# Performance work log

Hardware: AMD Instinct MI355X
Metric: run time of the kernel (lower is better)

The kernel has to match this reference:

```python
import jax, jax.numpy as jnp
import numpy as np

NUM_CLASSES = [5, 7, 4, 6, 3, 8, 5, 4, 6, 7, 3, 5, 4, 6, 8, 5, 7, 4, 6, 3]
N_ONE_HOTS = 20
N_OTHERS = 30
H = 48
W = 48
B = 128
N_MAP = 32
ENC_OUT = 32
RES_C = 128
OH_EMB = 9
SUM_NC = sum(NUM_CLASSES)  # 106


def conv2d(x, w, b=None, pad=0):
    # x: NCHW, w: OIHW
    y = jax.lax.conv_general_dilated(
        x, w, window_strides=(1, 1), padding=[(pad, pad), (pad, pad)],
        dimension_numbers=('NCHW', 'OIHW', 'NCHW'))
    if b is not None:
        y = y + b[None, :, None, None]
    return y


def setup_inputs() -> dict:
    key = jax.random.key(0)
    ks = jax.random.split(key, 20)
    x = jax.random.normal(ks[0], (B, 1 + N_MAP, H, W), dtype=jnp.float32)
    # first N_ONE_HOTS entries of flattened channel 0 are categorical indices
    idx_cols = [jax.random.randint(jax.random.fold_in(ks[1], j), (B,), 0, nc)
                for j, nc in enumerate(NUM_CLASSES)]
    idx = jnp.stack(idx_cols, axis=1).astype(jnp.float32)  # (B, 20)
    x = x.at[:, 0, 0, :N_ONE_HOTS].set(idx)
    s = 0.05
    inp = {
        'x': x,
        'fc_w': jax.random.normal(ks[2], (OH_EMB, SUM_NC), jnp.float32) * s,
        'fc_b': jnp.zeros((OH_EMB,), jnp.float32),
        'oh_conv_w': jax.random.normal(ks[3], (OH_EMB, OH_EMB, 1, 1), jnp.float32) * s,
        'oh_conv_b': jnp.zeros((OH_EMB,), jnp.float32),
        'others_conv_w': jax.random.normal(ks[4], (N_OTHERS, N_OTHERS, 1, 1), jnp.float32) * s,
        'others_conv_b': jnp.zeros((N_OTHERS,), jnp.float32),
        'all_conv_w': jax.random.normal(ks[5], (ENC_OUT, OH_EMB + N_OTHERS, 1, 1), jnp.float32) * s,
        'all_conv_b': jnp.zeros((ENC_OUT,), jnp.float32),
        'conv1_w': jax.random.normal(ks[6], (RES_C, ENC_OUT + N_MAP, 1, 1), jnp.float32) * s,
        'conv1_b': jnp.zeros((RES_C,), jnp.float32),
        'rconv1_w': jax.random.normal(ks[7], (RES_C, RES_C, 5, 5), jnp.float32) * s,
        'rconv1_b': jnp.zeros((RES_C,), jnp.float32),
        'rconv2_w': jax.random.normal(ks[8], (RES_C, RES_C, 5, 5), jnp.float32) * s,
        'rconv2_b': jnp.zeros((RES_C,), jnp.float32),
        'se_w1': jax.random.normal(ks[9], (RES_C // 16, RES_C), jnp.float32) * s,
        'se_w2': jax.random.normal(ks[10], (RES_C, RES_C // 16), jnp.float32) * s,
    }
    return inp


def reference(x, fc_w, fc_b, oh_conv_w, oh_conv_b, others_conv_w, others_conv_b,
              all_conv_w, all_conv_b, conv1_w, conv1_b, rconv1_w, rconv1_b,
              rconv2_w, rconv2_b, se_w1, se_w2):
    b = x.shape[0]
    gi = x[:, 0].reshape(b, -1)                 # (b, H*W)
    map_feature = x[:, 1:]                      # (b, N_MAP, H, W)
    idx = jax.lax.stop_gradient(gi[:, :N_ONE_HOTS]).astype(jnp.int32)
    others = gi[:, N_ONE_HOTS:N_ONE_HOTS + N_OTHERS]   # (b, 30)
    # vectorized one-hot build (replaces the quadratic python loop)
    oh = jnp.concatenate(
        [jax.nn.one_hot(idx[:, j], nc, dtype=x.dtype) for j, nc in enumerate(NUM_CLASSES)],
        axis=1)                                 # (b, SUM_NC)
    v = oh @ fc_w.T + fc_b                      # (b, 9)
    # faithful torch expand((h,w)+shape).reshape((b,-1,h,w)) semantics
    v = jnp.broadcast_to(v, (H, W, b, OH_EMB)).reshape(b, OH_EMB, H, W)
    o = jnp.broadcast_to(others, (H, W, b, N_OTHERS)).reshape(b, N_OTHERS, H, W)
    v = conv2d(v, oh_conv_w, oh_conv_b)
    o = conv2d(o, others_conv_w, others_conv_b)
    gi_map = conv2d(jnp.concatenate([v, o], axis=1), all_conv_w, all_conv_b)  # (b, 32, H, W)
    h = conv2d(jnp.concatenate([gi_map, map_feature], axis=1), conv1_w, conv1_b)  # (b, 128, H, W)
    # residual block: 5x5 convs, LeakyReLU, SE, identity skip (in==out)
    identity = h
    y = jax.nn.leaky_relu(conv2d(h, rconv1_w, rconv1_b, pad=2))
    y = conv2d(y, rconv2_w, rconv2_b, pad=2)
    s = y.mean(axis=(2, 3))                     # (b, 128)
    s = jax.nn.sigmoid(jax.nn.relu(s @ se_w1.T) @ se_w2.T)
    y = y * s[:, :, None, None]
    return jax.nn.leaky_relu(y + identity)
```

## Files before the change

kernel.cpp:

```cpp
#include <hip/hip_runtime.h>
#include <hip/hip_bf16.h>
#include <cstddef>

#define HH 48
#define WW 48
#define PIX 2304
#define PPIX 2704
#define BB 128
#define RESC 128
#define XCH 33

typedef short bf16x8 __attribute__((ext_vector_type(8)));
typedef float f32x4 __attribute__((ext_vector_type(4)));

static __device__ __forceinline__ float b2f(unsigned short u) {
    unsigned x = ((unsigned)u) << 16;
    return __builtin_bit_cast(float, x);
}
static __device__ __forceinline__ unsigned short f2b(float f) {
    __hip_bfloat16 hb = __float2bfloat16(f);
    return __builtin_bit_cast(unsigned short, hb);
}

#define GLOAD_LDS16(gp, lp) __builtin_amdgcn_global_load_lds( \
    (const __attribute__((address_space(1))) void*)(gp), \
    (__attribute__((address_space(3))) void*)(lp), 16, 0, 0)

__global__ void k_compute_v(const float* __restrict__ x, const float* __restrict__ fc_w,
                            const float* __restrict__ fc_b, float* __restrict__ v) {
    int b = blockIdx.x * blockDim.x + threadIdx.x;
    if (b >= BB) return;
    const int off[20] = {0,5,12,16,22,25,33,38,42,48,55,58,63,67,73,81,86,93,97,103};
    const float* gi = x + (size_t)b * XCH * PIX;
    int cols[20];
    #pragma unroll
    for (int j = 0; j < 20; j++) cols[j] = off[j] + (int)gi[j];
    #pragma unroll
    for (int e = 0; e < 9; e++) {
        float acc = fc_b[e];
        #pragma unroll
        for (int j = 0; j < 20; j++) acc += fc_w[e * 106 + cols[j]];
        v[b * 9 + e] = acc;
    }
}

__global__ void k_compute_G(const float* __restrict__ x, const float* __restrict__ v,
                            const float* __restrict__ ohw, const float* __restrict__ ohb,
                            const float* __restrict__ otw, const float* __restrict__ otb,
                            const float* __restrict__ aw,  const float* __restrict__ ab,
                            const float* __restrict__ c1w, const float* __restrict__ c1b,
                            float* __restrict__ G) {
    int p = blockIdx.x * blockDim.x + threadIdx.x;
    if (p >= PIX) return;
    float sv = v[((p / 9) & 127) * 9 + (p % 9)];
    float om[30];
    #pragma unroll
    for (int c2 = 0; c2 < 30; c2++) {
        int tmp = c2 * 24 + p;
        int c = tmp % 30;
        int bb = (c2 * 76 + tmp / 30) & 127;
        om[c2] = x[(size_t)bb * XCH * PIX + 20 + c];
    }
    float v9[9];
    #pragma unroll
    for (int e = 0; e < 9; e++) {
        float srow = 0.f;
        #pragma unroll
        for (int e2 = 0; e2 < 9; e2++) srow += ohw[e * 9 + e2];
        v9[e] = ohb[e] + srow * sv;
    }
    float o30[30];
    #pragma unroll
    for (int c = 0; c < 30; c++) {
        float a = otb[c];
        #pragma unroll
        for (int c2 = 0; c2 < 30; c2++) a += otw[c * 30 + c2] * om[c2];
        o30[c] = a;
    }
    float gi32[32];
    #pragma unroll
    for (int g = 0; g < 32; g++) {
        float a = ab[g];
        #pragma unroll
        for (int e = 0; e < 9; e++) a += aw[g * 39 + e] * v9[e];
        #pragma unroll
        for (int c = 0; c < 30; c++) a += aw[g * 39 + 9 + c] * o30[c];
        gi32[g] = a;
    }
    for (int oc = 0; oc < 128; oc++) {
        float a = c1b[oc];
        #pragma unroll
        for (int g = 0; g < 32; g++) a += c1w[oc * 64 + g] * gi32[g];
        G[p * 128 + oc] = a;
    }
}

__global__ void k_convert_w(const float* __restrict__ w1, const float* __restrict__ w2,
                            __hip_bfloat16* __restrict__ wb1, __hip_bfloat16* __restrict__ wb2) {
    int i = blockIdx.x * 256 + threadIdx.x;
    if (i >= 25 * 128 * 128) return;
    int tap = i / 16384, r = i % 16384;
    int oc = r >> 7, ic = r & 127;
    size_t src = (size_t)(oc * 128 + ic) * 25 + tap;
    wb1[i] = __float2bfloat16(w1[src]);
    wb2[i] = __float2bfloat16(w2[src]);
}

__global__ void k_zero_border(__hip_bfloat16* __restrict__ a, __hip_bfloat16* __restrict__ b2) {
    int img = blockIdx.x, t = threadIdx.x;
    for (int j = t; j < 6400; j += 256) {
        int pb = j >> 4, c16 = j & 15;
        int y, x2;
        if (pb < 208) { int q = pb / 52; y = q < 2 ? q : q + 48; x2 = pb % 52; }
        else { int r = pb - 208; y = 2 + (r >> 2); int c = r & 3; x2 = c < 2 ? c : c + 48; }
        size_t off = ((size_t)img * PPIX + y * 52 + x2) * 128 + c16 * 8;
        uint4 z = {0, 0, 0, 0};
        *(uint4*)(a + off) = z;
        *(uint4*)(b2 + off) = z;
    }
}

__global__ __launch_bounds__(256) void k_conv1(const float* __restrict__ x, const float* __restrict__ c1w,
                                               const float* __restrict__ G, __hip_bfloat16* __restrict__ h) {
    __shared__ float xm[32][64];
    __shared__ float w1[32][128];
    int b = blockIdx.y, p0 = blockIdx.x * 64;
    int t = threadIdx.x;
    for (int i = t; i < 4096; i += 256) { int m = i >> 7, oc = i & 127; w1[m][oc] = c1w[oc * 64 + 32 + m]; }
    for (int i = t; i < 2048; i += 256) {
        int m = i >> 6, pix = i & 63;
        xm[m][pix] = x[(size_t)b * XCH * PIX + (size_t)(1 + m) * PIX + p0 + pix];
    }
    __syncthreads();
    int pix = t & 63, ocg = t >> 6;
    float acc[32] = {};
    for (int m = 0; m < 32; m++) {
        float xv = xm[m][pix];
        const float4* wr = (const float4*)&w1[m][ocg * 32];
        #pragma unroll
        for (int k4 = 0; k4 < 8; k4++) {
            float4 wv = wr[k4];
            acc[k4 * 4 + 0] += wv.x * xv; acc[k4 * 4 + 1] += wv.y * xv;
            acc[k4 * 4 + 2] += wv.z * xv; acc[k4 * 4 + 3] += wv.w * xv;
        }
    }
    int p = p0 + pix;
    int py = p / 48, px2 = p % 48;
    size_t hb = ((size_t)b * PPIX + (py + 2) * 52 + px2 + 2) * 128 + ocg * 32;
    const float* gp = &G[(size_t)p * 128 + ocg * 32];
    #pragma unroll
    for (int q = 0; q < 4; q++) {
        unsigned short u[8];
        #pragma unroll
        for (int j = 0; j < 8; j++) u[j] = f2b(acc[q * 8 + j] + gp[q * 8 + j]);
        *(uint4*)(&h[hb + q * 8]) = *(uint4*)u;
    }
}

template<bool LEAKY, bool MEAN, bool PADOUT>
__global__ __launch_bounds__(256, 2) void k_conv5_mfma(
        const __hip_bfloat16* __restrict__ in,
        const __hip_bfloat16* __restrict__ w,
        const float* __restrict__ bias,
        __hip_bfloat16* __restrict__ out,
        float* __restrict__ mean) {
    __shared__ __align__(16) char lds[2][25600];
    int b = blockIdx.z, tile = blockIdx.x;
    int ty0 = (tile / 3) * 16, tx0 = (tile % 3) * 16;
    int t = threadIdx.x, lane = t & 63, wave = t >> 6;
    int wm = wave & 1, wn = wave >> 1;
    int l15 = lane & 15, lg = lane >> 4;

    const size_t inb = (size_t)b * PPIX * 128;
    const __hip_bfloat16* wbase = w + (size_t)(wm * 64 + l15) * 128 + lg * 8;

    int sbase[8];
    #pragma unroll
    for (int n = 0; n < 8; ++n) sbase[n] = (wn * 8 + n) * 20 + l15;

    f32x4 acc[4][8] = {};

    auto stage = [&](int buf, int icb2) {
        #pragma unroll
        for (int k = 0; k < 6; ++k) {
            int sg = k * 256 + t;
            int u = sg >> 3, j = sg & 7;
            int bb = j ^ (u & 7);
            int s = (u << 1) | (bb >> 2);
            int lg2 = bb & 3;
            int ry = s / 20, rx = s % 20;
            const __hip_bfloat16* gp = in + inb + (size_t)((ty0 + ry) * 52 + tx0 + rx) * 128 + icb2 + lg2 * 8;
            char* lp = &lds[buf][(k * 256 + (wave << 6)) * 16];
            GLOAD_LDS16(gp, lp);
        }
        if (wave == 0) {
            int sg = 1536 + lane;
            int u = sg >> 3, j = sg & 7;
            int bb = j ^ (u & 7);
            int s = (u << 1) | (bb >> 2);
            int lg2 = bb & 3;
            int ry = s / 20, rx = s % 20;
            const __hip_bfloat16* gp = in + inb + (size_t)((ty0 + ry) * 52 + tx0 + rx) * 128 + icb2 + lg2 * 8;
            char* lp = &lds[buf][1536 * 16];
            GLOAD_LDS16(gp, lp);
        }
    };

#define AISSUE(Areg, tap_) do { \
        const __hip_bfloat16* wp = wbase + (size_t)(tap_) * 16384 + icb; \
        Areg[0] = *(const bf16x8*)(wp); \
        Areg[1] = *(const bf16x8*)(wp + 2048); \
        Areg[2] = *(const bf16x8*)(wp + 4096); \
        Areg[3] = *(const bf16x8*)(wp + 6144); \
    } while (0)

#define CTAP(Areg, tap_) do { \
        int toff = (tap_) + 15 * ((tap_) / 5); \
        __builtin_amdgcn_s_setprio(1); \
        _Pragma("unroll") \
        for (int n = 0; n < 8; ++n) { \
            int s = sbase[n] + toff; \
            int u = s >> 1; \
            int jj = (((s & 1) << 2) | lg) ^ (u & 7); \
            bf16x8 Bv = *(const bf16x8*)(cb + (u << 7) + (jj << 4)); \
            acc[0][n] = __builtin_amdgcn_mfma_f32_16x16x32_bf16(Areg[0], Bv, acc[0][n], 0, 0, 0); \
            acc[1][n] = __builtin_amdgcn_mfma_f32_16x16x32_bf16(Areg[1], Bv, acc[1][n], 0, 0, 0); \
            acc[2][n] = __builtin_amdgcn_mfma_f32_16x16x32_bf16(Areg[2], Bv, acc[2][n], 0, 0, 0); \
            acc[3][n] = __builtin_amdgcn_mfma_f32_16x16x32_bf16(Areg[3], Bv, acc[3][n], 0, 0, 0); \
        } \
        __builtin_amdgcn_s_setprio(0); \
    } while (0)

    stage(0, 0);
    __syncthreads();

    for (int c = 0; c < 4; ++c) {
        const int icb = c * 32;
        const char* cb = lds[c & 1];
        bf16x8 A0[4], A1[4];
        AISSUE(A0, 0);
        AISSUE(A1, 1);
        __builtin_amdgcn_sched_barrier(0);
        if (c < 3) stage((c + 1) & 1, icb + 32);
        __builtin_amdgcn_sched_barrier(0);
        for (int i = 0; i < 12; ++i) {
            int tp = 2 * i;
            CTAP(A0, tp);
            AISSUE(A0, tp + 2);
            CTAP(A1, tp + 1);
            AISSUE(A1, tp + 3);
        }
        CTAP(A0, 24);
        if (c < 3) __syncthreads();
    }
#undef AISSUE
#undef CTAP

    #pragma unroll
    for (int m = 0; m < 4; ++m) {
        int ocm = wm * 64 + m * 16 + lg * 4;
        float b0 = bias[ocm], b1 = bias[ocm + 1], b2 = bias[ocm + 2], b3 = bias[ocm + 3];
        float ps0 = 0, ps1 = 0, ps2 = 0, ps3 = 0;
        #pragma unroll
        for (int n = 0; n < 8; ++n) {
            float v0 = acc[m][n][0] + b0, v1 = acc[m][n][1] + b1;
            float v2 = acc[m][n][2] + b2, v3 = acc[m][n][3] + b3;
            ps0 += v0; ps1 += v1; ps2 += v2; ps3 += v3;
            if (LEAKY) {
                v0 = v0 > 0.f ? v0 : 0.01f * v0; v1 = v1 > 0.f ? v1 : 0.01f * v1;
                v2 = v2 > 0.f ? v2 : 0.01f * v2; v3 = v3 > 0.f ? v3 : 0.01f * v3;
            }
            int row = ty0 + wn * 8 + n, col = tx0 + l15;
            size_t off;
            if (PADOUT) off = ((size_t)b * PPIX + (row + 2) * 52 + col + 2) * 128 + ocm;
            else        off = ((size_t)b * PIX + row * 48 + col) * 128 + ocm;
            uint2 pk;
            pk.x = (unsigned)f2b(v0) | ((unsigned)f2b(v1) << 16);
            pk.y = (unsigned)f2b(v2) | ((unsigned)f2b(v3) << 16);
            *(uint2*)(out + off) = pk;
        }
        if (MEAN) {
            #pragma unroll
            for (int mask = 1; mask < 16; mask <<= 1) {
                ps0 += __shfl_xor(ps0, mask);
                ps1 += __shfl_xor(ps1, mask);
                ps2 += __shfl_xor(ps2, mask);
                ps3 += __shfl_xor(ps3, mask);
            }
            if (l15 == 0) {
                atomicAdd(&mean[b * 128 + ocm], ps0);
                atomicAdd(&mean[b * 128 + ocm + 1], ps1);
                atomicAdd(&mean[b * 128 + ocm + 2], ps2);
                atomicAdd(&mean[b * 128 + ocm + 3], ps3);
            }
        }
    }
}

__global__ void k_se(const float* __restrict__ mean, const float* __restrict__ w1,
                     const float* __restrict__ w2, float* __restrict__ s) {
    __shared__ float m[128];
    __shared__ float tt[8];
    int b = blockIdx.x, t = threadIdx.x;
    m[t] = mean[b * RESC + t] * (1.0f / 2304.0f);
    __syncthreads();
    if (t < 8) {
        float a = 0.f;
        for (int i = 0; i < 128; i++) a += w1[t * 128 + i] * m[i];
        tt[t] = a > 0.f ? a : 0.f;
    }
    __syncthreads();
    float a = 0.f;
    #pragma unroll
    for (int r = 0; r < 8; r++) a += w2[t * 8 + r] * tt[r];
    s[b * RESC + t] = 1.f / (1.f + expf(-a));
}

__global__ __launch_bounds__(256) void k_final(const __hip_bfloat16* __restrict__ y2,
                                               const __hip_bfloat16* __restrict__ h,
                                               const float* __restrict__ sg, float* __restrict__ out) {
    __shared__ float sl[128];
    __shared__ float tile[64 * 129];
    int b = blockIdx.y, p0 = blockIdx.x * 64, t = threadIdx.x;
    if (t < 128) sl[t] = sg[b * 128 + t];
    __syncthreads();
    #pragma unroll
    for (int k = 0; k < 4; ++k) {
        int j = t + k * 256;
        int pix = j >> 4, c = j & 15;
        int p = p0 + pix;
        int py = p / 48, px2 = p % 48;
        uint4 yv = *(const uint4*)(y2 + ((size_t)b * PIX + p) * 128 + c * 8);
        uint4 hv = *(const uint4*)(h + ((size_t)b * PPIX + (py + 2) * 52 + px2 + 2) * 128 + c * 8);
        const unsigned short* yp = (const unsigned short*)&yv;
        const unsigned short* hp = (const unsigned short*)&hv;
        #pragma unroll
        for (int jj = 0; jj < 8; ++jj) {
            int oc = c * 8 + jj;
            tile[pix * 129 + oc] = b2f(yp[jj]) * sl[oc] + b2f(hp[jj]);
        }
    }
    __syncthreads();
    int oc = t >> 1, xh = (t & 1) * 32;
    float ov[32];
    #pragma unroll
    for (int i = 0; i < 32; ++i) {
        float v = tile[(xh + i) * 129 + oc];
        ov[i] = v > 0.f ? v : 0.01f * v;
    }
    float* op = out + ((size_t)b * 128 + oc) * PIX + p0 + xh;
    #pragma unroll
    for (int q = 0; q < 8; ++q) ((float4*)op)[q] = *(float4*)&ov[q * 4];
}

extern "C" void kernel_launch(void* const* d_in, const int* in_sizes, int n_in,
                              void* d_out, int out_size, void* d_ws, size_t ws_size,
                              hipStream_t stream) {
    const float* x      = (const float*)d_in[0];
    const float* fc_w   = (const float*)d_in[1];
    const float* fc_b   = (const float*)d_in[2];
    const float* ohw    = (const float*)d_in[3];
    const float* ohb    = (const float*)d_in[4];
    const float* otw    = (const float*)d_in[5];
    const float* otb    = (const float*)d_in[6];
    const float* aw     = (const float*)d_in[7];
    const float* ab     = (const float*)d_in[8];
    const float* c1w    = (const float*)d_in[9];
    const float* c1b    = (const float*)d_in[10];
    const float* r1w    = (const float*)d_in[11];
    const float* r1b    = (const float*)d_in[12];
    const float* r2w    = (const float*)d_in[13];
    const float* r2b    = (const float*)d_in[14];
    const float* se_w1  = (const float*)d_in[15];
    const float* se_w2  = (const float*)d_in[16];

    const size_t padb = (size_t)BB * PPIX * 128 * sizeof(__hip_bfloat16);
    char* ws = (char*)d_ws;
    __hip_bfloat16* h    = (__hip_bfloat16*)ws;  ws += padb;
    __hip_bfloat16* y1   = (__hip_bfloat16*)ws;  ws += padb;
    __hip_bfloat16* y2   = (__hip_bfloat16*)ws;  ws += (size_t)BB * PIX * 128 * sizeof(__hip_bfloat16);
    float* G    = (float*)ws;                    ws += (size_t)PIX * 128 * sizeof(float);
    float* v    = (float*)ws;                    ws += (size_t)BB * 9 * sizeof(float);
    __hip_bfloat16* wb1 = (__hip_bfloat16*)ws;   ws += (size_t)25 * 128 * 128 * sizeof(__hip_bfloat16);
    __hip_bfloat16* wb2 = (__hip_bfloat16*)ws;   ws += (size_t)25 * 128 * 128 * sizeof(__hip_bfloat16);
    ws += 131072;
    float* mean = (float*)ws;                    ws += (size_t)BB * RESC * sizeof(float);
    float* sgate= (float*)ws;                    ws += (size_t)BB * RESC * sizeof(float);

    k_compute_v<<<1, 128, 0, stream>>>(x, fc_w, fc_b, v);
    k_compute_G<<<9, 256, 0, stream>>>(x, v, ohw, ohb, otw, otb, aw, ab, c1w, c1b, G);
    k_convert_w<<<1600, 256, 0, stream>>>(r1w, r2w, wb1, wb2);
    k_zero_border<<<128, 256, 0, stream>>>(h, y1);
    k_conv1<<<dim3(36, 128), 256, 0, stream>>>(x, c1w, G, h);
    k_conv5_mfma<true, false, true><<<dim3(9, 1, 128), 256, 0, stream>>>(h, wb1, r1b, y1, nullptr);
    hipMemsetAsync(mean, 0, (size_t)BB * RESC * sizeof(float), stream);
    k_conv5_mfma<false, true, false><<<dim3(9, 1, 128), 256, 0, stream>>>(y1, wb2, r2b, y2, mean);
    k_se<<<128, 128, 0, stream>>>(mean, se_w1, se_w2, sgate);
    k_final<<<dim3(36, 128), 256, 0, stream>>>(y2, h, sgate, (float*)d_out);
}
```

Measured before the change: 812.8 us.

## Halve conv5 spatial tile to 8x16 and raise occupancy to four blocks

Result: slower. 1.562 ms (+92.2%).

```diff
diff --git a/kernel.cpp b/kernel.cpp
--- a/kernel.cpp
+++ b/kernel.cpp
@@ -158,103 +158,79 @@
 }
 
 template<bool LEAKY, bool MEAN, bool PADOUT>
-__global__ __launch_bounds__(256, 2) void k_conv5_mfma(
+__global__ __launch_bounds__(256, 4) void k_conv5_mfma(
         const __hip_bfloat16* __restrict__ in,
         const __hip_bfloat16* __restrict__ w,
         const float* __restrict__ bias,
         __hip_bfloat16* __restrict__ out,
         float* __restrict__ mean) {
-    __shared__ __align__(16) char lds[2][25600];
+    __shared__ __align__(16) char lds[2 * 15360];
     int b = blockIdx.z, tile = blockIdx.x;
-    int ty0 = (tile / 3) * 16, tx0 = (tile % 3) * 16;
+    int ty0 = (tile / 3) * 8, tx0 = (tile % 3) * 16;
     int t = threadIdx.x, lane = t & 63, wave = t >> 6;
-    int wm = wave & 1, wn = wave >> 1;
+    int wm = wave & 1, wp = wave >> 1;
     int l15 = lane & 15, lg = lane >> 4;
 
     const size_t inb = (size_t)b * PPIX * 128;
-    const __hip_bfloat16* wbase = w + (size_t)(wm * 64 + l15) * 128 + lg * 8;
-
-    int sbase[8];
-    #pragma unroll
-    for (int n = 0; n < 8; ++n) sbase[n] = (wn * 8 + n) * 20 + l15;
-
-    f32x4 acc[4][8] = {};
+    const int wrow = (wm * 64 + l15) * 128 + lg * 8;
+
+    int sbase[4];
+    #pragma unroll
+    for (int n = 0; n < 4; ++n) sbase[n] = (wp * 4 + n) * 20 + l15;
+
+    f32x4 acc[4][4] = {};
 
     auto stage = [&](int buf, int icb2) {
         #pragma unroll
-        for (int k = 0; k < 6; ++k) {
-            int sg = k * 256 + t;
-            int u = sg >> 3, j = sg & 7;
-            int bb = j ^ (u & 7);
-            int s = (u << 1) | (bb >> 2);
-            int lg2 = bb & 3;
-            int ry = s / 20, rx = s % 20;
-            const __hip_bfloat16* gp = in + inb + (size_t)((ty0 + ry) * 52 + tx0 + rx) * 128 + icb2 + lg2 * 8;
-            char* lp = &lds[buf][(k * 256 + (wave << 6)) * 16];
-            GLOAD_LDS16(gp, lp);
-        }
-        if (wave == 0) {
-            int sg = 1536 + lane;
-            int u = sg >> 3, j = sg & 7;
-            int bb = j ^ (u & 7);
-            int s = (u << 1) | (bb >> 2);
-            int lg2 = bb & 3;
-            int ry = s / 20, rx = s % 20;
-            const __hip_bfloat16* gp = in + inb + (size_t)((ty0 + ry) * 52 + tx0 + rx) * 128 + icb2 + lg2 * 8;
-            char* lp = &lds[buf][1536 * 16];
-            GLOAD_LDS16(gp, lp);
+        for (int k = 0; k < 4; ++k) {
+            if (k < 3 || t < 192) {
+                int sg = k * 256 + t;
+                int u = sg >> 3, j = sg & 7;
+                int bb = j ^ (u & 7);
+                int s = (u << 1) | (bb >> 2);
+                int lg2 = bb & 3;
+                int ry = s / 20, rx = s % 20;
+                const __hip_bfloat16* gp = in + inb + (size_t)((ty0 + ry) * 52 + tx0 + rx) * 128 + icb2 + lg2 * 8;
+                char* lp = lds + buf * 15360 + sg * 16;
+                GLOAD_LDS16(gp, lp);
+            }
         }
     };
 
-#define AISSUE(Areg, tap_) do { \
-        const __hip_bfloat16* wp = wbase + (size_t)(tap_) * 16384 + icb; \
-        Areg[0] = *(const bf16x8*)(wp); \
-        Areg[1] = *(const bf16x8*)(wp + 2048); \
-        Areg[2] = *(const bf16x8*)(wp + 4096); \
-        Areg[3] = *(const bf16x8*)(wp + 6144); \
-    } while (0)
-
-#define CTAP(Areg, tap_) do { \
-        int toff = (tap_) + 15 * ((tap_) / 5); \
-        __builtin_amdgcn_s_setprio(1); \
-        _Pragma("unroll") \
-        for (int n = 0; n < 8; ++n) { \
-            int s = sbase[n] + toff; \
-            int u = s >> 1; \
-            int jj = (((s & 1) << 2) | lg) ^ (u & 7); \
-            bf16x8 Bv = *(const bf16x8*)(cb + (u << 7) + (jj << 4)); \
-            acc[0][n] = __builtin_amdgcn_mfma_f32_16x16x32_bf16(Areg[0], Bv, acc[0][n], 0, 0, 0); \
-            acc[1][n] = __builtin_amdgcn_mfma_f32_16x16x32_bf16(Areg[1], Bv, acc[1][n], 0, 0, 0); \
-            acc[2][n] = __builtin_amdgcn_mfma_f32_16x16x32_bf16(Areg[2], Bv, acc[2][n], 0, 0, 0); \
-            acc[3][n] = __builtin_amdgcn_mfma_f32_16x16x32_bf16(Areg[3], Bv, acc[3][n], 0, 0, 0); \
-        } \
-        __builtin_amdgcn_s_setprio(0); \
-    } while (0)
-
     stage(0, 0);
     __syncthreads();
 
+    #pragma unroll 1
     for (int c = 0; c < 4; ++c) {
         const int icb = c * 32;
-        const char* cb = lds[c & 1];
-        bf16x8 A0[4], A1[4];
-        AISSUE(A0, 0);
-        AISSUE(A1, 1);
-        __builtin_amdgcn_sched_barrier(0);
-        if (c < 3) stage((c + 1) & 1, icb + 32);
-        __builtin_amdgcn_sched_barrier(0);
-        for (int i = 0; i < 12; ++i) {
-            int tp = 2 * i;
-            CTAP(A0, tp);
-            AISSUE(A0, tp + 2);
-            CTAP(A1, tp + 1);
-            AISSUE(A1, tp + 3);
-        }
-        CTAP(A0, 24);
+        const char* cb = lds + (c & 1) * 15360;
+        #pragma unroll
+        for (int dy = 0; dy < 5; ++dy) {
+            #pragma unroll
+            for (int dx = 0; dx < 5; ++dx) {
+                const __hip_bfloat16* wt = w + (size_t)(dy * 5 + dx) * 16384 + wrow + icb;
+                bf16x8 A0 = *(const bf16x8*)(wt);
+                bf16x8 A1 = *(const bf16x8*)(wt + 2048);
+                bf16x8 A2 = *(const bf16x8*)(wt + 4096);
+                bf16x8 A3 = *(const bf16x8*)(wt + 6144);
+                if (dy == 0 && dx == 2 && c < 3) stage((c + 1) & 1, icb + 32);
+                __builtin_amdgcn_s_setprio(1);
+                #pragma unroll
+                for (int n = 0; n < 4; ++n) {
+                    int s = sbase[n] + dy * 20 + dx;
+                    int u = s >> 1;
+                    int jj = (((s & 1) << 2) | lg) ^ (u & 7);
+                    bf16x8 Bv = *(const bf16x8*)(cb + (u << 7) + (jj << 4));
+                    acc[0][n] = __builtin_amdgcn_mfma_f32_16x16x32_bf16(A0, Bv, acc[0][n], 0, 0, 0);
+                    acc[1][n] = __builtin_amdgcn_mfma_f32_16x16x32_bf16(A1, Bv, acc[1][n], 0, 0, 0);
+                    acc[2][n] = __builtin_amdgcn_mfma_f32_16x16x32_bf16(A2, Bv, acc[2][n], 0, 0, 0);
+                    acc[3][n] = __builtin_amdgcn_mfma_f32_16x16x32_bf16(A3, Bv, acc[3][n], 0, 0, 0);
+                }
+                __builtin_amdgcn_s_setprio(0);
+            }
+        }
         if (c < 3) __syncthreads();
     }
-#undef AISSUE
-#undef CTAP
 
     #pragma unroll
     for (int m = 0; m < 4; ++m) {
@@ -262,7 +238,7 @@
         float b0 = bias[ocm], b1 = bias[ocm + 1], b2 = bias[ocm + 2], b3 = bias[ocm + 3];
         float ps0 = 0, ps1 = 0, ps2 = 0, ps3 = 0;
         #pragma unroll
-        for (int n = 0; n < 8; ++n) {
+        for (int n = 0; n < 4; ++n) {
             float v0 = acc[m][n][0] + b0, v1 = acc[m][n][1] + b1;
             float v2 = acc[m][n][2] + b2, v3 = acc[m][n][3] + b3;
             ps0 += v0; ps1 += v1; ps2 += v2; ps3 += v3;
@@ -270,7 +246,7 @@
                 v0 = v0 > 0.f ? v0 : 0.01f * v0; v1 = v1 > 0.f ? v1 : 0.01f * v1;
                 v2 = v2 > 0.f ? v2 : 0.01f * v2; v3 = v3 > 0.f ? v3 : 0.01f * v3;
             }
-            int row = ty0 + wn * 8 + n, col = tx0 + l15;
+            int row = ty0 + wp * 4 + n, col = tx0 + l15;
             size_t off;
             if (PADOUT) off = ((size_t)b * PPIX + (row + 2) * 52 + col + 2) * 128 + ocm;
             else        off = ((size_t)b * PIX + row * 48 + col) * 128 + ocm;
@@ -383,7 +359,6 @@
     float* v    = (float*)ws;                    ws += (size_t)BB * 9 * sizeof(float);
     __hip_bfloat16* wb1 = (__hip_bfloat16*)ws;   ws += (size_t)25 * 128 * 128 * sizeof(__hip_bfloat16);
     __hip_bfloat16* wb2 = (__hip_bfloat16*)ws;   ws += (size_t)25 * 128 * 128 * sizeof(__hip_bfloat16);
-    ws += 131072;
     float* mean = (float*)ws;                    ws += (size_t)BB * RESC * sizeof(float);
     float* sgate= (float*)ws;                    ws += (size_t)BB * RESC * sizeof(float);
 
@@ -392,9 +367,9 @@
     k_convert_w<<<1600, 256, 0, stream>>>(r1w, r2w, wb1, wb2);
     k_zero_border<<<128, 256, 0, stream>>>(h, y1);
     k_conv1<<<dim3(36, 128), 256, 0, stream>>>(x, c1w, G, h);
-    k_conv5_mfma<true, false, true><<<dim3(9, 1, 128), 256, 0, stream>>>(h, wb1, r1b, y1, nullptr);
+    k_conv5_mfma<true, false, true><<<dim3(18, 1, 128), 256, 0, stream>>>(h, wb1, r1b, y1, nullptr);
     hipMemsetAsync(mean, 0, (size_t)BB * RESC * sizeof(float), stream);
-    k_conv5_mfma<false, true, false><<<dim3(9, 1, 128), 256, 0, stream>>>(y1, wb2, r2b, y2, mean);
+    k_conv5_mfma<false, true, false><<<dim3(18, 1, 128), 256, 0, stream>>>(y1, wb2, r2b, y2, mean);
     k_se<<<128, 128, 0, stream>>>(mean, se_w1, se_w2, sgate);
     k_final<<<dim3(36, 128), 256, 0, stream>>>(y2, h, sgate, (float*)d_out);
 }
```

## Process two batch images per conv5 block and prefetch LDS B operands

Applied to the files above, without the earlier changes.

Measured after the change: 932.0 us. +14.7%, slower.

```diff
diff --git a/kernel.cpp b/kernel.cpp
--- a/kernel.cpp
+++ b/kernel.cpp
@@ -158,51 +158,46 @@
 }
 
 template<bool LEAKY, bool MEAN, bool PADOUT>
-__global__ __launch_bounds__(256, 2) void k_conv5_mfma(
+__global__ __launch_bounds__(512, 2) void k_conv5_mfma(
         const __hip_bfloat16* __restrict__ in,
         const __hip_bfloat16* __restrict__ w,
         const float* __restrict__ bias,
         __hip_bfloat16* __restrict__ out,
         float* __restrict__ mean) {
-    __shared__ __align__(16) char lds[2][25600];
-    int b = blockIdx.z, tile = blockIdx.x;
+    __shared__ __align__(16) char lds[2 * 51200];
+    int b0 = blockIdx.z * 2, tile = blockIdx.x;
     int ty0 = (tile / 3) * 16, tx0 = (tile % 3) * 16;
     int t = threadIdx.x, lane = t & 63, wave = t >> 6;
     int wm = wave & 1, wn = wave >> 1;
+    int wb = wn >> 1, wr = wn & 1;
     int l15 = lane & 15, lg = lane >> 4;
 
-    const size_t inb = (size_t)b * PPIX * 128;
+    const size_t inb = (size_t)(b0 + wb) * PPIX * 128;
     const __hip_bfloat16* wbase = w + (size_t)(wm * 64 + l15) * 128 + lg * 8;
 
     int sbase[8];
     #pragma unroll
-    for (int n = 0; n < 8; ++n) sbase[n] = (wn * 8 + n) * 20 + l15;
+    for (int n = 0; n < 8; ++n) sbase[n] = (wr * 8 + n) * 20 + l15;
 
     f32x4 acc[4][8] = {};
 
     auto stage = [&](int buf, int icb2) {
         #pragma unroll
-        for (int k = 0; k < 6; ++k) {
-            int sg = k * 256 + t;
-            int u = sg >> 3, j = sg & 7;
-            int bb = j ^ (u & 7);
-            int s = (u << 1) | (bb >> 2);
-            int lg2 = bb & 3;
-            int ry = s / 20, rx = s % 20;
-            const __hip_bfloat16* gp = in + inb + (size_t)((ty0 + ry) * 52 + tx0 + rx) * 128 + icb2 + lg2 * 8;
-            char* lp = &lds[buf][(k * 256 + (wave << 6)) * 16];
-            GLOAD_LDS16(gp, lp);
-        }
-        if (wave == 0) {
-            int sg = 1536 + lane;
-            int u = sg >> 3, j = sg & 7;
-            int bb = j ^ (u & 7);
-            int s = (u << 1) | (bb >> 2);
-            int lg2 = bb & 3;
-            int ry = s / 20, rx = s % 20;
-            const __hip_bfloat16* gp = in + inb + (size_t)((ty0 + ry) * 52 + tx0 + rx) * 128 + icb2 + lg2 * 8;
-            char* lp = &lds[buf][1536 * 16];
-            GLOAD_LDS16(gp, lp);
+        for (int k = 0; k < 7; ++k) {
+            if (k < 6 || t < 128) {
+                int sg = k * 512 + t;
+                int bsel = sg >= 1600;
+                int ul = sg - bsel * 1600;
+                int u = ul >> 3, j = ul & 7;
+                int bb = j ^ (u & 7);
+                int s = (u << 1) | (bb >> 2);
+                int lg2 = bb & 3;
+                int ry = s / 20, rx = s % 20;
+                const __hip_bfloat16* gp = in + (size_t)(b0 + bsel) * PPIX * 128
+                    + (size_t)((ty0 + ry) * 52 + tx0 + rx) * 128 + icb2 + lg2 * 8;
+                char* lp = lds + buf * 51200 + sg * 16;
+                GLOAD_LDS16(gp, lp);
+            }
         }
     };
 
@@ -214,19 +209,22 @@
         Areg[3] = *(const bf16x8*)(wp + 6144); \
     } while (0)
 
+#define LDSB(s_) (*(const bf16x8*)(cb + (((s_) >> 1) << 7) + \
+        (((((s_) & 1) << 2) | lg) ^ (((s_) >> 1) & 7)) * 16))
+
 #define CTAP(Areg, tap_) do { \
         int toff = (tap_) + 15 * ((tap_) / 5); \
+        bf16x8 Bcur = LDSB(sbase[0] + toff); \
         __builtin_amdgcn_s_setprio(1); \
         _Pragma("unroll") \
         for (int n = 0; n < 8; ++n) { \
-            int s = sbase[n] + toff; \
-            int u = s >> 1; \
-            int jj = (((s & 1) << 2) | lg) ^ (u & 7); \
-            bf16x8 Bv = *(const bf16x8*)(cb + (u << 7) + (jj << 4)); \
-            acc[0][n] = __builtin_amdgcn_mfma_f32_16x16x32_bf16(Areg[0], Bv, acc[0][n], 0, 0, 0); \
-            acc[1][n] = __builtin_amdgcn_mfma_f32_16x16x32_bf16(Areg[1], Bv, acc[1][n], 0, 0, 0); \
-            acc[2][n] = __builtin_amdgcn_mfma_f32_16x16x32_bf16(Areg[2], Bv, acc[2][n], 0, 0, 0); \
-            acc[3][n] = __builtin_amdgcn_mfma_f32_16x16x32_bf16(Areg[3], Bv, acc[3][n], 0, 0, 0); \
+            bf16x8 Bnxt = Bcur; \
+            if (n < 7) Bnxt = LDSB(sbase[n + 1] + toff); \
+            acc[0][n] = __builtin_amdgcn_mfma_f32_16x16x32_bf16(Areg[0], Bcur, acc[0][n], 0, 0, 0); \
+            acc[1][n] = __builtin_amdgcn_mfma_f32_16x16x32_bf16(Areg[1], Bcur, acc[1][n], 0, 0, 0); \
+            acc[2][n] = __builtin_amdgcn_mfma_f32_16x16x32_bf16(Areg[2], Bcur, acc[2][n], 0, 0, 0); \
+            acc[3][n] = __builtin_amdgcn_mfma_f32_16x16x32_bf16(Areg[3], Bcur, acc[3][n], 0, 0, 0); \
+            Bcur = Bnxt; \
         } \
         __builtin_amdgcn_s_setprio(0); \
     } while (0)
@@ -236,7 +234,7 @@
 
     for (int c = 0; c < 4; ++c) {
         const int icb = c * 32;
-        const char* cb = lds[c & 1];
+        const char* cb = lds + (c & 1) * 51200 + wb * 25600;
         bf16x8 A0[4], A1[4];
         AISSUE(A0, 0);
         AISSUE(A1, 1);
@@ -254,26 +252,28 @@
         if (c < 3) __syncthreads();
     }
 #undef AISSUE
+#undef LDSB
 #undef CTAP
 
+    const int bo = b0 + wb;
     #pragma unroll
     for (int m = 0; m < 4; ++m) {
         int ocm = wm * 64 + m * 16 + lg * 4;
-        float b0 = bias[ocm], b1 = bias[ocm + 1], b2 = bias[ocm + 2], b3 = bias[ocm + 3];
+        float bv0 = bias[ocm], bv1 = bias[ocm + 1], bv2 = bias[ocm + 2], bv3 = bias[ocm + 3];
         float ps0 = 0, ps1 = 0, ps2 = 0, ps3 = 0;
         #pragma unroll
         for (int n = 0; n < 8; ++n) {
-            float v0 = acc[m][n][0] + b0, v1 = acc[m][n][1] + b1;
-            float v2 = acc[m][n][2] + b2, v3 = acc[m][n][3] + b3;
+            float v0 = acc[m][n][0] + bv0, v1 = acc[m][n][1] + bv1;
+            float v2 = acc[m][n][2] + bv2, v3 = acc[m][n][3] + bv3;
             ps0 += v0; ps1 += v1; ps2 += v2; ps3 += v3;
             if (LEAKY) {
                 v0 = v0 > 0.f ? v0 : 0.01f * v0; v1 = v1 > 0.f ? v1 : 0.01f * v1;
                 v2 = v2 > 0.f ? v2 : 0.01f * v2; v3 = v3 > 0.f ? v3 : 0.01f * v3;
             }
-            int row = ty0 + wn * 8 + n, col = tx0 + l15;
+            int row = ty0 + wr * 8 + n, col = tx0 + l15;
             size_t off;
-            if (PADOUT) off = ((size_t)b * PPIX + (row + 2) * 52 + col + 2) * 128 + ocm;
-            else        off = ((size_t)b * PIX + row * 48 + col) * 128 + ocm;
+            if (PADOUT) off = ((size_t)bo * PPIX + (row + 2) * 52 + col + 2) * 128 + ocm;
+            else        off = ((size_t)bo * PIX + row * 48 + col) * 128 + ocm;
             uint2 pk;
             pk.x = (unsigned)f2b(v0) | ((unsigned)f2b(v1) << 16);
             pk.y = (unsigned)f2b(v2) | ((unsigned)f2b(v3) << 16);
@@ -288,10 +288,10 @@
                 ps3 += __shfl_xor(ps3, mask);
             }
             if (l15 == 0) {
-                atomicAdd(&mean[b * 128 + ocm], ps0);
-                atomicAdd(&mean[b * 128 + ocm + 1], ps1);
-                atomicAdd(&mean[b * 128 + ocm + 2], ps2);
-                atomicAdd(&mean[b * 128 + ocm + 3], ps3);
+                atomicAdd(&mean[bo * 128 + ocm], ps0);
+                atomicAdd(&mean[bo * 128 + ocm + 1], ps1);
+                atomicAdd(&mean[bo * 128 + ocm + 2], ps2);
+                atomicAdd(&mean[bo * 128 + ocm + 3], ps3);
             }
         }
     }
@@ -392,9 +392,9 @@
     k_convert_w<<<1600, 256, 0, stream>>>(r1w, r2w, wb1, wb2);
     k_zero_border<<<128, 256, 0, stream>>>(h, y1);
     k_conv1<<<dim3(36, 128), 256, 0, stream>>>(x, c1w, G, h);
-    k_conv5_mfma<true, false, true><<<dim3(9, 1, 128), 256, 0, stream>>>(h, wb1, r1b, y1, nullptr);
+    k_conv5_mfma<true, false, true><<<dim3(9, 1, 64), 512, 0, stream>>>(h, wb1, r1b, y1, nullptr);
     hipMemsetAsync(mean, 0, (size_t)BB * RESC * sizeof(float), stream);
-    k_conv5_mfma<false, true, false><<<dim3(9, 1, 128), 256, 0, stream>>>(y1, wb2, r2b, y2, mean);
+    k_conv5_mfma<false, true, false><<<dim3(9, 1, 64), 512, 0, stream>>>(y1, wb2, r2b, y2, mean);
     k_se<<<128, 128, 0, stream>>>(mean, se_w1, se_w2, sgate);
     k_final<<<dim3(36, 128), 256, 0, stream>>>(y2, h, sgate, (float*)d_out);
 }
```
